# Kernel tuning notes

Measured on AMD Instinct MI355X. Metric: run time of the kernel, lower is better.

The kernel has to match this reference:

```python
import jax, jax.numpy as jnp
import numpy as np

P = 100_000      # distinct products
T = 300_000      # total product nodes after repeat_interleave (sum of cnt)
NQ = 100_000     # query nodes
B = 8192         # number of sessions (segments)
QIN = 128; PIN = 128; D = 128; MSL = 50; DL = D - MSL


def setup_inputs() -> dict:
    key = jax.random.key(0)
    ks = jax.random.split(key, 12)
    # irregular repeat counts in {1..5}, tiled so sum == 3*P == T exactly (static shape)
    cnt = jnp.asarray(np.tile(np.array([1, 2, 3, 4, 5], np.int32), P // 5))
    s = 0.05
    return {
        "query_feat": jax.random.normal(ks[0], (NQ, QIN), jnp.float32),
        "product_feat": jax.random.normal(ks[1], (P, PIN), jnp.float32),
        "Wq": jax.random.normal(ks[2], (DL, QIN), jnp.float32) * s,
        "bq": jnp.zeros((DL,), jnp.float32),
        "Wp": jax.random.normal(ks[3], (DL, PIN), jnp.float32) * s,
        "bp": jnp.zeros((DL,), jnp.float32),
        "pos_table": jax.random.normal(ks[4], (MSL, MSL), jnp.float32) * s,
        "Wn": jax.random.normal(ks[5], (D, D), jnp.float32) * s,
        "bn": jnp.zeros((D,), jnp.float32),
        "Wc": jax.random.normal(ks[6], (D, D), jnp.float32) * s,
        "Wa": jax.random.normal(ks[7], (1, D), jnp.float32) * s,
        "query_pos_id": jax.random.randint(ks[8], (NQ,), 0, MSL, jnp.int32),
        "product_pos_id": jax.random.randint(ks[9], (T,), 0, MSL, jnp.int32),
        "query_batch": jax.random.randint(ks[10], (NQ,), 0, B, jnp.int32),
        "product_batch": jax.random.randint(ks[11], (P,), 0, B, jnp.int32),
        "cnt": cnt,
        "num_segments": B,
        "total_product_nodes": T,
    }


def _segment_mean(x, seg, num_segments):
    sums = jax.ops.segment_sum(x, seg, num_segments=num_segments)
    counts = jax.ops.segment_sum(jnp.ones((x.shape[0],), x.dtype), seg, num_segments=num_segments)
    return sums / jnp.maximum(counts, 1.0)[:, None]


def reference(query_feat, product_feat, Wq, bq, Wp, bp, pos_table, Wn, bn, Wc, Wa,
              query_pos_id, product_pos_id, query_batch, product_batch, cnt,
              num_segments, total_product_nodes):
    # query branch: linear -> concat positional embedding -> tanh  [NQ, D]
    qe = jnp.tanh(jnp.concatenate([query_feat @ Wq.T + bq, pos_table[query_pos_id]], axis=1))
    # product branch: linear, repeat_interleave by cnt, concat pos emb, tanh  [T, D]
    pe = product_feat @ Wp.T + bp
    pe = jnp.repeat(pe, cnt, axis=0, total_repeat_length=total_product_nodes)
    pe = jnp.tanh(jnp.concatenate([pe, pos_table[product_pos_id]], axis=1))
    pbatch = jnp.repeat(product_batch, cnt, axis=0, total_repeat_length=total_product_nodes)
    # stack nodes (products first, then queries — matches torch.concat order)
    node_emb = jnp.concatenate([pe, qe], axis=0)            # [N, D]
    node_batch = jnp.concatenate([pbatch, query_batch], axis=0)
    # coarse session representation: segment mean, broadcast back to nodes
    coarse = _segment_mean(node_emb, node_batch, num_segments)  # [B, D]
    coarse_g = coarse[node_batch]                                # [N, D]
    # attention gating
    att = jax.nn.sigmoid(node_emb @ Wn.T + bn + coarse_g @ Wc.T) @ Wa.T  # [N, 1]
    weighted = node_emb * att
    return _segment_mean(weighted, node_batch, num_segments)    # [B, D]
```

## Files before the change

### kernel.cpp

```cpp
#include <hip/hip_runtime.h>
#include <hip/hip_bf16.h>
#include <math.h>


constexpr int D   = 128;
constexpr int DL  = 78;
constexpr int MSL = 50;
constexpr int RP  = 80;

typedef __attribute__((ext_vector_type(8))) short bfrag8;
typedef __attribute__((ext_vector_type(4))) float facc4;
typedef __attribute__((ext_vector_type(4))) short short4v;

__device__ __forceinline__ float sigmoidf_(float x) {
    return 1.f / (1.f + __expf(-x));
}
__device__ __forceinline__ float ftanh(float x) {
    float e = __expf(2.f * x);
    return 1.f - 2.f * __builtin_amdgcn_rcpf(e + 1.f);
}
__device__ __forceinline__ float bs2f(short s) {
    unsigned u = ((unsigned)(unsigned short)s) << 16;
    return __builtin_bit_cast(float, u);
}
__device__ __forceinline__ short f2bs(float f) {
    return __builtin_bit_cast(short, __float2bfloat16(f));
}

__device__ __forceinline__ char* ldsAddr(__hip_bfloat16* base, int row, int byte_in_row) {
    return reinterpret_cast<char*>(base) + row * 256 + (byte_in_row ^ ((row & 7) << 4));
}
__device__ __forceinline__ bfrag8 ldsR16(const __hip_bfloat16* base, int row, int byte_in_row) {
    return *reinterpret_cast<const bfrag8*>(
        reinterpret_cast<const char*>(base) + row * 256 + (byte_in_row ^ ((row & 7) << 4)));
}
__device__ __forceinline__ short4v ldsR8(const __hip_bfloat16* base, int row, int byte_in_row) {
    return *reinterpret_cast<const short4v*>(
        reinterpret_cast<const char*>(base) + row * 256 + (byte_in_row ^ ((row & 7) << 4)));
}

__device__ __forceinline__ bfrag8 cvt8(float4 a, float4 b) {
    __hip_bfloat16 t[8] = {__float2bfloat16(a.x), __float2bfloat16(a.y),
                           __float2bfloat16(a.z), __float2bfloat16(a.w),
                           __float2bfloat16(b.x), __float2bfloat16(b.y),
                           __float2bfloat16(b.z), __float2bfloat16(b.w)};
    return *reinterpret_cast<bfrag8*>(t);
}

__global__ __launch_bounds__(256) void k_tables2(
    const float* __restrict__ pos_table, const float* __restrict__ Wn,
    float* __restrict__ tpos, __hip_bfloat16* __restrict__ posWnbf) {
    __shared__ float tposL[MSL * MSL];
    int t = threadIdx.x;
    for (int o = t; o < MSL * MSL; o += 256) tposL[o] = tanhf(pos_table[o]);
    __syncthreads();
    if (blockIdx.x == 0)
        for (int o = t; o < MSL * MSL; o += 256) tpos[o] = tposL[o];
    for (int o = blockIdx.x * 256 + t; o < MSL * D; o += gridDim.x * 256) {
        int r = o >> 7, d = o & 127;
        float acc = 0.f;
        #pragma unroll 10
        for (int j = 0; j < MSL; ++j) acc += tposL[r * MSL + j] * Wn[d * D + DL + j];
        posWnbf[o] = __float2bfloat16(acc);
    }
}

__global__ __launch_bounds__(256) void k_convW(
    const float* __restrict__ Wq, const float* __restrict__ Wp, const float* __restrict__ Wn,
    const float* __restrict__ Wa,
    __hip_bfloat16* __restrict__ Wqbf, __hip_bfloat16* __restrict__ Wpbf,
    __hip_bfloat16* __restrict__ Wnbf, __hip_bfloat16* __restrict__ Wabf) {
    int i = blockIdx.x * 256 + threadIdx.x;
    if (i < 80 * 128) {
        int n = i >> 7;
        Wqbf[i] = __float2bfloat16((n < DL) ? Wq[i] : 0.f);
        Wpbf[i] = __float2bfloat16((n < DL) ? Wp[i] : 0.f);
    } else if (i < 80 * 128 + 128 * 128) {
        int o = i - 80 * 128;
        int j = o & 127;
        Wnbf[o] = __float2bfloat16((j < DL) ? Wn[o] : 0.f);
    } else if (i < 80 * 128 + 128 * 128 + 128) {
        int o = i - 80 * 128 - 128 * 128;
        Wabf[o] = __float2bfloat16(Wa[o]);
    }
}

__global__ void k_scanA(const int* __restrict__ cnt, int P, int* __restrict__ chunkSum) {
    __shared__ int s[256];
    int p = blockIdx.x * 256 + threadIdx.x;
    s[threadIdx.x] = (p < P) ? cnt[p] : 0;
    __syncthreads();
    for (int st = 128; st > 0; st >>= 1) {
        if (threadIdx.x < st) s[threadIdx.x] += s[threadIdx.x + st];
        __syncthreads();
    }
    if (threadIdx.x == 0) chunkSum[blockIdx.x] = s[0];
}
__global__ __launch_bounds__(1024) void k_scanB(
    const int* __restrict__ chunkSum, int nC, int* __restrict__ chunkOff) {
    __shared__ int s[1024];
    int t = threadIdx.x;
    int carry = 0;
    for (int base = 0; base < nC; base += 1024) {
        int v = (base + t < nC) ? chunkSum[base + t] : 0;
        s[t] = v;
        __syncthreads();
        for (int st = 1; st < 1024; st <<= 1) {
            int add = (t >= st) ? s[t - st] : 0;
            __syncthreads();
            s[t] += add;
            __syncthreads();
        }
        if (base + t < nC) chunkOff[base + t] = carry + s[t] - v;
        carry += s[1023];
        __syncthreads();
    }
}
__global__ void k_scanC(const int* __restrict__ cnt, int P, const int* __restrict__ chunkOff,
                        int* __restrict__ prodOff) {
    __shared__ int s[256];
    int t = threadIdx.x;
    int p = blockIdx.x * 256 + t;
    int v = (p < P) ? cnt[p] : 0;
    s[t] = v;
    __syncthreads();
    for (int st = 1; st < 256; st <<= 1) {
        int add = (t >= st) ? s[t - st] : 0;
        __syncthreads();
        s[t] += add;
        __syncthreads();
    }
    if (p < P) prodOff[p] = chunkOff[blockIdx.x] + s[t] - v;
}

__global__ void k_cnt2(const int* __restrict__ qbatch, const int* __restrict__ pbatch,
                       const int* __restrict__ cnt, int NQ, int P, int* __restrict__ nodeCnt) {
    int i = blockIdx.x * 256 + threadIdx.x;
    if (i < NQ) {
        atomicAdd(&nodeCnt[qbatch[i]], 1);
    } else if (i < NQ + P) {
        int p = i - NQ;
        atomicAdd(&nodeCnt[pbatch[p]], cnt[p]);
    }
}
__global__ __launch_bounds__(1024) void k_scanSeg(
    const int* __restrict__ nodeCnt, int B, int* __restrict__ segOff, int* __restrict__ cursor) {
    __shared__ int s[1024];
    int t = threadIdx.x;
    int carry = 0;
    for (int base = 0; base < B; base += 1024) {
        int v = (base + t < B) ? nodeCnt[base + t] : 0;
        s[t] = v;
        __syncthreads();
        for (int st = 1; st < 1024; st <<= 1) {
            int add = (t >= st) ? s[t - st] : 0;
            __syncthreads();
            s[t] += add;
            __syncthreads();
        }
        if (base + t < B) {
            int e = carry + s[t] - v;
            segOff[base + t] = e;
            cursor[base + t] = e;
        }
        carry += s[1023];
        __syncthreads();
    }
    if (t == 0) segOff[B] = carry;
}
__global__ void k_rank2(const int* __restrict__ qbatch, const int* __restrict__ pbatch,
                        const int* __restrict__ qpos, const int* __restrict__ ppos,
                        const int* __restrict__ cnt, const int* __restrict__ prodOff,
                        int NQ, int P, int* __restrict__ cursor,
                        int* __restrict__ nodeIdx, int* __restrict__ nodeSeg) {
    int i = blockIdx.x * 256 + threadIdx.x;
    if (i < NQ) {
        int b = qbatch[i];
        int slot = atomicAdd(&cursor[b], 1);
        nodeIdx[slot] = (i << 6) | qpos[i];
        nodeSeg[slot] = b;
    } else if (i < NQ + P) {
        int p = i - NQ;
        int b = pbatch[p];
        int c = cnt[p], off = prodOff[p];
        int slot = atomicAdd(&cursor[b], c);
        for (int j = 0; j < c; ++j) {
            nodeIdx[slot + j] = ((NQ + p) << 6) | ppos[off + j];
            nodeSeg[slot + j] = b;
        }
    }
}

__global__ __launch_bounds__(256) void k_branch2(
    const float* __restrict__ qfeat, const float* __restrict__ pfeat,
    const __hip_bfloat16* __restrict__ Wqbf, const __hip_bfloat16* __restrict__ Wpbf,
    const float* __restrict__ bq, const float* __restrict__ bp,
    const __hip_bfloat16* __restrict__ Wnbf,
    int NQ, int P, int qBlocks,
    __hip_bfloat16* __restrict__ tEU, __hip_bfloat16* __restrict__ eWnU) {
    const bool isQ = (int)blockIdx.x < qBlocks;
    const int r0 = (isQ ? blockIdx.x : blockIdx.x - qBlocks) * 64;
    const float* feat = isQ ? qfeat : pfeat;
    const __hip_bfloat16* Wbf = isQ ? Wqbf : Wpbf;
    const float* bias = isQ ? bq : bp;
    const int Nrows = isQ ? NQ : P;
    const int rowBase = isQ ? 0 : NQ;

    __shared__ __hip_bfloat16 linL[64 * 128];
    __shared__ __hip_bfloat16 eWnL[64 * 128];
    int t = threadIdx.x;
    int l = t & 63, w = t >> 6;
    int lr = l & 15, lq = l >> 4;
    int am = w * 16 + lr;

    if (l < 16) {
        bfrag8 z = {0, 0, 0, 0, 0, 0, 0, 0};
        *reinterpret_cast<bfrag8*>(ldsAddr(linL, w * 16 + l, 160)) = z;
        *reinterpret_cast<bfrag8*>(ldsAddr(linL, w * 16 + l, 176)) = z;
    }

    int gra = r0 + am;
    const float* frow = &feat[(size_t)(gra < Nrows ? gra : Nrows - 1) * 128];
    bfrag8 a[4];
    #pragma unroll
    for (int kt = 0; kt < 4; ++kt) {
        float4 u = *reinterpret_cast<const float4*>(&frow[kt * 32 + lq * 8]);
        float4 v = *reinterpret_cast<const float4*>(&frow[kt * 32 + lq * 8 + 4]);
        a[kt] = cvt8(u, v);
    }

    facc4 c1[5];
    #pragma unroll
    for (int nt = 0; nt < 5; ++nt) { facc4 z = {0.f, 0.f, 0.f, 0.f}; c1[nt] = z; }
    #pragma unroll
    for (int nt = 0; nt < 5; ++nt) {
        #pragma unroll
        for (int kt = 0; kt < 4; ++kt) {
            bfrag8 b = *reinterpret_cast<const bfrag8*>(&Wbf[(nt * 16 + lr) * 128 + kt * 32 + lq * 8]);
            c1[nt] = __builtin_amdgcn_mfma_f32_16x16x32_bf16(a[kt], b, c1[nt], 0, 0, 0);
        }
    }

    #pragma unroll
    for (int nt = 0; nt < 5; ++nt) {
        int n = nt * 16 + lr;
        float bs = (n < DL) ? bias[n] : 0.f;
        #pragma unroll
        for (int j = 0; j < 4; ++j) {
            int m = w * 16 + lq * 4 + j;
            float tv = (n < DL) ? ftanh(c1[nt][j] + bs) : 0.f;
            *reinterpret_cast<__hip_bfloat16*>(ldsAddr(linL, m, 2 * n)) = __float2bfloat16(tv);
        }
    }

    {
        int r = w * 16 + (l >> 2), c = l & 3;
        int gr = r0 + r;
        #pragma unroll
        for (int j = 0; j < 5; ++j) {
            short4v v = ldsR8(linL, r, c * 40 + j * 8);
            if (gr < Nrows)
                *reinterpret_cast<short4v*>(&tEU[(size_t)(rowBase + gr) * RP + c * 20 + j * 4]) = v;
        }
    }

    bfrag8 a2[3];
    #pragma unroll
    for (int kt = 0; kt < 3; ++kt) a2[kt] = ldsR16(linL, am, kt * 64 + lq * 16);
    facc4 c2[8];
    #pragma unroll
    for (int nt = 0; nt < 8; ++nt) { facc4 z = {0.f, 0.f, 0.f, 0.f}; c2[nt] = z; }
    #pragma unroll
    for (int nt = 0; nt < 8; ++nt) {
        #pragma unroll
        for (int kt = 0; kt < 3; ++kt) {
            bfrag8 b = *reinterpret_cast<const bfrag8*>(&Wnbf[(nt * 16 + lr) * 128 + kt * 32 + lq * 8]);
            c2[nt] = __builtin_amdgcn_mfma_f32_16x16x32_bf16(a2[kt], b, c2[nt], 0, 0, 0);
        }
    }
    #pragma unroll
    for (int nt = 0; nt < 8; ++nt) {
        int d2 = nt * 16 + lr;
        #pragma unroll
        for (int j = 0; j < 4; ++j) {
            int m = w * 16 + lq * 4 + j;
            *reinterpret_cast<__hip_bfloat16*>(ldsAddr(eWnL, m, 2 * d2)) =
                __float2bfloat16(c2[nt][j]);
        }
    }
    {
        int r = w * 16 + (l >> 2), c = l & 3;
        int gr = r0 + r;
        #pragma unroll
        for (int j = 0; j < 4; ++j) {
            bfrag8 v = ldsR16(eWnL, r, c * 64 + j * 16);
            if (gr < Nrows)
                *reinterpret_cast<bfrag8*>(&eWnU[(size_t)(rowBase + gr) * 128 + c * 32 + j * 8]) = v;
        }
    }
}

__global__ __launch_bounds__(128) void k_segsum3(
    const __hip_bfloat16* __restrict__ tEU, const int* __restrict__ nodeIdx,
    const int* __restrict__ segOff, const float* __restrict__ tpos, int B,
    float* __restrict__ segsum, float* __restrict__ segcnt) {
    int b = blockIdx.x, t = threadIdx.x;
    int s0 = segOff[b], s1 = segOff[b + 1];
    float acc = 0.f;
    if (t < DL) {
        for (int i = s0; i < s1; i += 4) {
            #pragma unroll
            for (int j = 0; j < 4; ++j) {
                if (i + j < s1) {
                    int row = nodeIdx[i + j] >> 6;
                    acc += __bfloat162float(tEU[(size_t)row * RP + t]);
                }
            }
        }
        segsum[(size_t)b * D + t] = acc;
    } else {
        int k = t - DL;
        for (int i = s0; i < s1; i += 4) {
            #pragma unroll
            for (int j = 0; j < 4; ++j) {
                if (i + j < s1) {
                    int pos = nodeIdx[i + j] & 63;
                    acc += tpos[pos * MSL + k];
                }
            }
        }
        segsum[(size_t)b * D + DL + k] = acc;
        if (k == 0) segcnt[b] = (float)(s1 - s0);
    }
}

__global__ __launch_bounds__(256) void k_coarse(
    const float* __restrict__ segsum, const float* __restrict__ segcnt,
    const float* __restrict__ Wc, const float* __restrict__ bn, int B,
    __hip_bfloat16* __restrict__ cWcbf) {
    __shared__ __hip_bfloat16 WcL[128 * 130];
    __shared__ float cL[16 * 128];
    int t = threadIdx.x;
    int b0 = blockIdx.x * 16;
    for (int o = t; o < D * D; o += 256) {
        int d = o >> 7, k = o & 127;
        WcL[d * 130 + k] = __float2bfloat16(Wc[o]);
    }
    for (int o = t; o < 16 * D; o += 256) {
        int bb = o >> 7, d = o & 127;
        int b = b0 + bb;
        cL[o] = (b < B) ? segsum[(size_t)b * D + d] / fmaxf(segcnt[b], 1.f) : 0.f;
    }
    __syncthreads();
    for (int o = t; o < 16 * D; o += 256) {
        int bb = o >> 7, d = o & 127;
        int b = b0 + bb;
        if (b >= B) continue;
        float acc = bn[d];
        const float* cr = &cL[bb * 128];
        const __hip_bfloat16* wr = &WcL[d * 130];
        #pragma unroll 8
        for (int j = 0; j < D; ++j) acc += cr[j] * __bfloat162float(wr[j]);
        cWcbf[(size_t)b * D + d] = __float2bfloat16(acc);
    }
}

__global__ __launch_bounds__(256) void k_attw(
    const __hip_bfloat16* __restrict__ eWnU, const __hip_bfloat16* __restrict__ cWcbf,
    const __hip_bfloat16* __restrict__ posWnbf, const __hip_bfloat16* __restrict__ Wabf,
    const int* __restrict__ nodeIdx, const int* __restrict__ nodeSeg,
    int NN, float* __restrict__ att) {
    int t = threadIdx.x;
    int l = t & 63, w = t >> 6;
    int lr = l & 15, lq = l >> 4;
    int i0 = blockIdx.x * 64 + w * 16;
    int n = i0 + lr;
    bool on = n < NN;
    int pk = on ? nodeIdx[n] : 0;
    int b  = on ? nodeSeg[n] : 0;
    int row = pk >> 6, pos = pk & 63;

    facc4 c = {0.f, 0.f, 0.f, 0.f};
    #pragma unroll
    for (int kt = 0; kt < 4; ++kt) {
        int col = kt * 32 + lq * 8;
        bfrag8 e  = *reinterpret_cast<const bfrag8*>(&eWnU[(size_t)row * D + col]);
        bfrag8 cw = *reinterpret_cast<const bfrag8*>(&cWcbf[(size_t)b * D + col]);
        bfrag8 pw = *reinterpret_cast<const bfrag8*>(&posWnbf[pos * D + col]);
        bfrag8 s;
        #pragma unroll
        for (int j = 0; j < 8; ++j) {
            float z = bs2f(e[j]) + bs2f(cw[j]) + bs2f(pw[j]);
            s[j] = f2bs(sigmoidf_(z));
        }
        bfrag8 wa = *reinterpret_cast<const bfrag8*>(&Wabf[col]);
        c = __builtin_amdgcn_mfma_f32_16x16x32_bf16(s, wa, c, 0, 0, 0);
    }
    if (lr == 0) {
        #pragma unroll
        for (int j = 0; j < 4; ++j) {
            int m = i0 + lq * 4 + j;
            if (m < NN) att[m] = c[j];
        }
    }
}

__global__ __launch_bounds__(256) void k_pool(
    const __hip_bfloat16* __restrict__ tEU, const float* __restrict__ att,
    const float* __restrict__ tpos, const int* __restrict__ nodeIdx,
    const int* __restrict__ segOff, const float* __restrict__ segcnt,
    int B, float* __restrict__ out) {
    int wv = threadIdx.x >> 6, l = threadIdx.x & 63;
    int b = blockIdx.x * 4 + wv;
    if (b >= B) return;
    int s0 = segOff[b], s1 = segOff[b + 1];
    float acc0 = 0.f, acc1 = 0.f;

    for (int i = s0; i < s1; i += 4) {
        float a[4];
        int row[4], pos[4];
        #pragma unroll
        for (int j = 0; j < 4; ++j) {
            bool on = (i + j) < s1;
            int pk = on ? nodeIdx[i + j] : 0;
            a[j] = on ? att[i + j] : 0.f;
            row[j] = pk >> 6;
            pos[j] = pk & 63;
        }
        #pragma unroll
        for (int j = 0; j < 4; ++j) {
            acc0 += a[j] * __bfloat162float(tEU[(size_t)row[j] * RP + l]);
            if (l < 14) acc1 += a[j] * __bfloat162float(tEU[(size_t)row[j] * RP + 64 + l]);
            else        acc1 += a[j] * tpos[pos[j] * MSL + (l - 14)];
        }
    }

    float inv = 1.f / fmaxf(segcnt[b], 1.f);
    out[(size_t)b * D + l] = acc0 * inv;
    out[(size_t)b * D + 64 + l] = acc1 * inv;
}

extern "C" void kernel_launch(void* const* d_in, const int* in_sizes, int n_in,
                              void* d_out, int out_size, void* d_ws, size_t ws_size,
                              hipStream_t stream) {
    const float* query_feat   = (const float*)d_in[0];
    const float* product_feat = (const float*)d_in[1];
    const float* Wq = (const float*)d_in[2];
    const float* bq = (const float*)d_in[3];
    const float* Wp = (const float*)d_in[4];
    const float* bp = (const float*)d_in[5];
    const float* pos_table = (const float*)d_in[6];
    const float* Wn = (const float*)d_in[7];
    const float* bn = (const float*)d_in[8];
    const float* Wc = (const float*)d_in[9];
    const float* Wa = (const float*)d_in[10];
    const int* qpos   = (const int*)d_in[11];
    const int* ppos   = (const int*)d_in[12];
    const int* qbatch = (const int*)d_in[13];
    const int* pbatch = (const int*)d_in[14];
    const int* cnt    = (const int*)d_in[15];

    int NQ = in_sizes[11];
    int T  = in_sizes[12];
    int P  = in_sizes[15];
    int B  = out_size / D;
    int NR = NQ + P;
    int NN = NQ + T;
    float* out = (float*)d_out;

    char* w = (char*)d_ws;
    size_t off = 0;
    auto take = [&](size_t bytes) -> char* {
        char* p = w + off;
        off = (off + bytes + 255) & ~(size_t)255;
        return p;
    };
    int*   nodeCnt = (int*)  take((size_t)B * 4);
    size_t zeroBytes = off;
    float* segsum   = (float*)take((size_t)B * D * 4);
    float* segcnt   = (float*)take((size_t)B * 4);
    float* tpos  = (float*)take(MSL * MSL * 4);
    __hip_bfloat16* posWnbf = (__hip_bfloat16*)take(MSL * D * 2);
    __hip_bfloat16* cWcbf   = (__hip_bfloat16*)take((size_t)B * D * 2);
    __hip_bfloat16* Wqbf = (__hip_bfloat16*)take(80 * 128 * 2);
    __hip_bfloat16* Wpbf = (__hip_bfloat16*)take(80 * 128 * 2);
    __hip_bfloat16* Wnbf = (__hip_bfloat16*)take(128 * 128 * 2);
    __hip_bfloat16* Wabf = (__hip_bfloat16*)take(128 * 2);
    int nC = (P + 255) / 256;
    int* chunkSum = (int*)take((size_t)nC * 4);
    int* chunkOff = (int*)take((size_t)nC * 4);
    int* prodOff  = (int*)take((size_t)P * 4);
    int* segOffA  = (int*)take((size_t)(B + 1) * 4);
    int* cursor   = (int*)take((size_t)B * 4);
    int* nodeIdx  = (int*)take((size_t)NN * 4);
    int* nodeSeg  = (int*)take((size_t)NN * 4);
    float* att    = (float*)take((size_t)NN * 4);
    __hip_bfloat16* tEU  = (__hip_bfloat16*)take((size_t)NR * RP * 2);
    __hip_bfloat16* eWnU = (__hip_bfloat16*)take((size_t)NR * D * 2);
    (void)ws_size; (void)n_in;

    hipMemsetAsync(nodeCnt, 0, zeroBytes, stream);

    hipLaunchKernelGGL(k_tables2, dim3(8), dim3(256), 0, stream, pos_table, Wn, tpos, posWnbf);
    hipLaunchKernelGGL(k_convW, dim3((80 * 128 + 128 * 128 + 128 + 255) / 256), dim3(256), 0,
                       stream, Wq, Wp, Wn, Wa, Wqbf, Wpbf, Wnbf, Wabf);
    hipLaunchKernelGGL(k_scanA, dim3(nC), dim3(256), 0, stream, cnt, P, chunkSum);
    hipLaunchKernelGGL(k_scanB, dim3(1), dim3(1024), 0, stream, chunkSum, nC, chunkOff);
    hipLaunchKernelGGL(k_scanC, dim3(nC), dim3(256), 0, stream, cnt, P, chunkOff, prodOff);

    hipLaunchKernelGGL(k_cnt2, dim3((NR + 255) / 256), dim3(256), 0, stream,
                       qbatch, pbatch, cnt, NQ, P, nodeCnt);
    hipLaunchKernelGGL(k_scanSeg, dim3(1), dim3(1024), 0, stream, nodeCnt, B, segOffA, cursor);
    hipLaunchKernelGGL(k_rank2, dim3((NR + 255) / 256), dim3(256), 0, stream,
                       qbatch, pbatch, qpos, ppos, cnt, prodOff, NQ, P, cursor,
                       nodeIdx, nodeSeg);

    int qBlocks = (NQ + 63) / 64, pBlocksBr = (P + 63) / 64;
    hipLaunchKernelGGL(k_branch2, dim3(qBlocks + pBlocksBr), dim3(256), 0, stream,
                       query_feat, product_feat, Wqbf, Wpbf, bq, bp, Wnbf,
                       NQ, P, qBlocks, tEU, eWnU);

    hipLaunchKernelGGL(k_segsum3, dim3(B), dim3(128), 0, stream,
                       tEU, nodeIdx, segOffA, tpos, B, segsum, segcnt);
    hipLaunchKernelGGL(k_coarse, dim3((B + 15) / 16), dim3(256), 0, stream,
                       segsum, segcnt, Wc, bn, B, cWcbf);

    hipLaunchKernelGGL(k_attw, dim3((NN + 63) / 64), dim3(256), 0, stream,
                       eWnU, cWcbf, posWnbf, Wabf, nodeIdx, nodeSeg, NN, att);
    hipLaunchKernelGGL(k_pool, dim3((B + 3) / 4), dim3(256), 0, stream,
                       tEU, att, tpos, nodeIdx, segOffA, segcnt, B, out);
}
```

Baseline: 322.8 us.

## Make branch kernel persistent with LDS-resident Wn and next-tile feature prefetch

The branch GEMM kernel becomes a persistent grid of 768 blocks that loops over 64-row tiles. Each block stages the bf16 Wn matrix in LDS once, and while the current tile computes it prefetches the next tile's fp32 feature rows into registers. A single LDS scratch buffer now replaces the separate linear and eWn buffers. The pooling kernel also unrolls its node loop from 4 to 8 to keep more gathers in flight. The aim is to amortise Wn loads and hide global feature-load latency, at the cost of more register pressure and fewer blocks in flight.

```diff
diff --git a/kernel.cpp b/kernel.cpp
--- a/kernel.cpp
+++ b/kernel.cpp
@@ -191,111 +191,145 @@
     }
 }
 
-__global__ __launch_bounds__(256) void k_branch2(
+__global__ __launch_bounds__(256) void k_branch3(
     const float* __restrict__ qfeat, const float* __restrict__ pfeat,
     const __hip_bfloat16* __restrict__ Wqbf, const __hip_bfloat16* __restrict__ Wpbf,
     const float* __restrict__ bq, const float* __restrict__ bp,
     const __hip_bfloat16* __restrict__ Wnbf,
-    int NQ, int P, int qBlocks,
+    int NQ, int P, int nTilesQ, int nTiles,
     __hip_bfloat16* __restrict__ tEU, __hip_bfloat16* __restrict__ eWnU) {
-    const bool isQ = (int)blockIdx.x < qBlocks;
-    const int r0 = (isQ ? blockIdx.x : blockIdx.x - qBlocks) * 64;
-    const float* feat = isQ ? qfeat : pfeat;
-    const __hip_bfloat16* Wbf = isQ ? Wqbf : Wpbf;
-    const float* bias = isQ ? bq : bp;
-    const int Nrows = isQ ? NQ : P;
-    const int rowBase = isQ ? 0 : NQ;
-
-    __shared__ __hip_bfloat16 linL[64 * 128];
-    __shared__ __hip_bfloat16 eWnL[64 * 128];
+    __shared__ __hip_bfloat16 sL[64 * 128];
+    __shared__ __hip_bfloat16 WnL[128 * 128];
+
     int t = threadIdx.x;
     int l = t & 63, w = t >> 6;
     int lr = l & 15, lq = l >> 4;
     int am = w * 16 + lr;
 
-    if (l < 16) {
-        bfrag8 z = {0, 0, 0, 0, 0, 0, 0, 0};
-        *reinterpret_cast<bfrag8*>(ldsAddr(linL, w * 16 + l, 160)) = z;
-        *reinterpret_cast<bfrag8*>(ldsAddr(linL, w * 16 + l, 176)) = z;
-    }
-
-    int gra = r0 + am;
-    const float* frow = &feat[(size_t)(gra < Nrows ? gra : Nrows - 1) * 128];
-    bfrag8 a[4];
-    #pragma unroll
-    for (int kt = 0; kt < 4; ++kt) {
-        float4 u = *reinterpret_cast<const float4*>(&frow[kt * 32 + lq * 8]);
-        float4 v = *reinterpret_cast<const float4*>(&frow[kt * 32 + lq * 8 + 4]);
-        a[kt] = cvt8(u, v);
-    }
-
-    facc4 c1[5];
-    #pragma unroll
-    for (int nt = 0; nt < 5; ++nt) { facc4 z = {0.f, 0.f, 0.f, 0.f}; c1[nt] = z; }
-    #pragma unroll
-    for (int nt = 0; nt < 5; ++nt) {
+    for (int i = t; i < 128 * 16; i += 256) {
+        int row = i >> 4, chunk = i & 15;
+        bfrag8 v = *reinterpret_cast<const bfrag8*>(&Wnbf[row * 128 + chunk * 8]);
+        *reinterpret_cast<bfrag8*>(ldsAddr(WnL, row, chunk * 16)) = v;
+    }
+    __syncthreads();
+
+    auto tileFrow = [&](int tl) -> const float* {
+        bool iq = tl < nTilesQ;
+        int r0 = (iq ? tl : tl - nTilesQ) * 64;
+        const float* f = iq ? qfeat : pfeat;
+        int Nr = iq ? NQ : P;
+        int gr = r0 + am;
+        return &f[(size_t)(gr < Nr ? gr : Nr - 1) * 128];
+    };
+
+    int tile = blockIdx.x;
+    float4 uN[4], vN[4];
+    if (tile < nTiles) {
+        const float* fr = tileFrow(tile);
         #pragma unroll
         for (int kt = 0; kt < 4; ++kt) {
-            bfrag8 b = *reinterpret_cast<const bfrag8*>(&Wbf[(nt * 16 + lr) * 128 + kt * 32 + lq * 8]);
-            c1[nt] = __builtin_amdgcn_mfma_f32_16x16x32_bf16(a[kt], b, c1[nt], 0, 0, 0);
-        }
-    }
-
-    #pragma unroll
-    for (int nt = 0; nt < 5; ++nt) {
-        int n = nt * 16 + lr;
-        float bs = (n < DL) ? bias[n] : 0.f;
-        #pragma unroll
-        for (int j = 0; j < 4; ++j) {
-            int m = w * 16 + lq * 4 + j;
-            float tv = (n < DL) ? ftanh(c1[nt][j] + bs) : 0.f;
-            *reinterpret_cast<__hip_bfloat16*>(ldsAddr(linL, m, 2 * n)) = __float2bfloat16(tv);
-        }
-    }
-
-    {
-        int r = w * 16 + (l >> 2), c = l & 3;
-        int gr = r0 + r;
-        #pragma unroll
-        for (int j = 0; j < 5; ++j) {
-            short4v v = ldsR8(linL, r, c * 40 + j * 8);
-            if (gr < Nrows)
-                *reinterpret_cast<short4v*>(&tEU[(size_t)(rowBase + gr) * RP + c * 20 + j * 4]) = v;
-        }
-    }
-
-    bfrag8 a2[3];
-    #pragma unroll
-    for (int kt = 0; kt < 3; ++kt) a2[kt] = ldsR16(linL, am, kt * 64 + lq * 16);
-    facc4 c2[8];
-    #pragma unroll
-    for (int nt = 0; nt < 8; ++nt) { facc4 z = {0.f, 0.f, 0.f, 0.f}; c2[nt] = z; }
-    #pragma unroll
-    for (int nt = 0; nt < 8; ++nt) {
-        #pragma unroll
-        for (int kt = 0; kt < 3; ++kt) {
-            bfrag8 b = *reinterpret_cast<const bfrag8*>(&Wnbf[(nt * 16 + lr) * 128 + kt * 32 + lq * 8]);
-            c2[nt] = __builtin_amdgcn_mfma_f32_16x16x32_bf16(a2[kt], b, c2[nt], 0, 0, 0);
-        }
-    }
-    #pragma unroll
-    for (int nt = 0; nt < 8; ++nt) {
-        int d2 = nt * 16 + lr;
-        #pragma unroll
-        for (int j = 0; j < 4; ++j) {
-            int m = w * 16 + lq * 4 + j;
-            *reinterpret_cast<__hip_bfloat16*>(ldsAddr(eWnL, m, 2 * d2)) =
-                __float2bfloat16(c2[nt][j]);
-        }
-    }
-    {
-        int r = w * 16 + (l >> 2), c = l & 3;
-        int gr = r0 + r;
-        #pragma unroll
-        for (int j = 0; j < 4; ++j) {
-            bfrag8 v = ldsR16(eWnL, r, c * 64 + j * 16);
-            if (gr < Nrows)
-                *reinterpret_cast<bfrag8*>(&eWnU[(size_t)(rowBase + gr) * 128 + c * 32 + j * 8]) = v;
+            uN[kt] = *reinterpret_cast<const float4*>(&fr[kt * 32 + lq * 8]);
+            vN[kt] = *reinterpret_cast<const float4*>(&fr[kt * 32 + lq * 8 + 4]);
+        }
+    }
+
+    for (; tile < nTiles; tile += gridDim.x) {
+        const bool isQ = tile < nTilesQ;
+        const int r0 = (isQ ? tile : tile - nTilesQ) * 64;
+        const __hip_bfloat16* Wbf = isQ ? Wqbf : Wpbf;
+        const float* bias = isQ ? bq : bp;
+        const int Nrows = isQ ? NQ : P;
+        const int rowBase = isQ ? 0 : NQ;
+
+        bfrag8 a[4];
+        #pragma unroll
+        for (int kt = 0; kt < 4; ++kt) a[kt] = cvt8(uN[kt], vN[kt]);
+
+        if (l < 16) {
+            bfrag8 z = {0, 0, 0, 0, 0, 0, 0, 0};
+            *reinterpret_cast<bfrag8*>(ldsAddr(sL, w * 16 + l, 160)) = z;
+            *reinterpret_cast<bfrag8*>(ldsAddr(sL, w * 16 + l, 176)) = z;
+        }
+
+        facc4 c1[5];
+        #pragma unroll
+        for (int nt = 0; nt < 5; ++nt) { facc4 z = {0.f, 0.f, 0.f, 0.f}; c1[nt] = z; }
+        #pragma unroll
+        for (int nt = 0; nt < 5; ++nt) {
+            #pragma unroll
+            for (int kt = 0; kt < 4; ++kt) {
+                bfrag8 b = *reinterpret_cast<const bfrag8*>(&Wbf[(nt * 16 + lr) * 128 + kt * 32 + lq * 8]);
+                c1[nt] = __builtin_amdgcn_mfma_f32_16x16x32_bf16(a[kt], b, c1[nt], 0, 0, 0);
+            }
+        }
+
+        int tnext = tile + gridDim.x;
+        if (tnext < nTiles) {
+            const float* fr = tileFrow(tnext);
+            #pragma unroll
+            for (int kt = 0; kt < 4; ++kt) {
+                uN[kt] = *reinterpret_cast<const float4*>(&fr[kt * 32 + lq * 8]);
+                vN[kt] = *reinterpret_cast<const float4*>(&fr[kt * 32 + lq * 8 + 4]);
+            }
+        }
+
+        #pragma unroll
+        for (int nt = 0; nt < 5; ++nt) {
+            int n = nt * 16 + lr;
+            float bs = (n < DL) ? bias[n] : 0.f;
+            #pragma unroll
+            for (int j = 0; j < 4; ++j) {
+                int m = w * 16 + lq * 4 + j;
+                float tv = (n < DL) ? ftanh(c1[nt][j] + bs) : 0.f;
+                *reinterpret_cast<__hip_bfloat16*>(ldsAddr(sL, m, 2 * n)) = __float2bfloat16(tv);
+            }
+        }
+
+        {
+            int r = w * 16 + (l >> 2), c = l & 3;
+            int gr = r0 + r;
+            #pragma unroll
+            for (int j = 0; j < 5; ++j) {
+                short4v v = ldsR8(sL, r, c * 40 + j * 8);
+                if (gr < Nrows)
+                    *reinterpret_cast<short4v*>(&tEU[(size_t)(rowBase + gr) * RP + c * 20 + j * 4]) = v;
+            }
+        }
+
+        bfrag8 a2[3];
+        #pragma unroll
+        for (int kt = 0; kt < 3; ++kt) a2[kt] = ldsR16(sL, am, kt * 64 + lq * 16);
+        facc4 c2[8];
+        #pragma unroll
+        for (int nt = 0; nt < 8; ++nt) { facc4 z = {0.f, 0.f, 0.f, 0.f}; c2[nt] = z; }
+        #pragma unroll
+        for (int nt = 0; nt < 8; ++nt) {
+            #pragma unroll
+            for (int kt = 0; kt < 3; ++kt) {
+                bfrag8 b = ldsR16(WnL, nt * 16 + lr, kt * 64 + lq * 16);
+                c2[nt] = __builtin_amdgcn_mfma_f32_16x16x32_bf16(a2[kt], b, c2[nt], 0, 0, 0);
+            }
+        }
+
+        #pragma unroll
+        for (int nt = 0; nt < 8; ++nt) {
+            int d2 = nt * 16 + lr;
+            #pragma unroll
+            for (int j = 0; j < 4; ++j) {
+                int m = w * 16 + lq * 4 + j;
+                *reinterpret_cast<__hip_bfloat16*>(ldsAddr(sL, m, 2 * d2)) =
+                    __float2bfloat16(c2[nt][j]);
+            }
+        }
+        {
+            int r = w * 16 + (l >> 2), c = l & 3;
+            int gr = r0 + r;
+            #pragma unroll
+            for (int j = 0; j < 4; ++j) {
+                bfrag8 v = ldsR16(sL, r, c * 64 + j * 16);
+                if (gr < Nrows)
+                    *reinterpret_cast<bfrag8*>(&eWnU[(size_t)(rowBase + gr) * 128 + c * 32 + j * 8]) = v;
+            }
         }
     }
 }
@@ -416,11 +450,11 @@
     int s0 = segOff[b], s1 = segOff[b + 1];
     float acc0 = 0.f, acc1 = 0.f;
 
-    for (int i = s0; i < s1; i += 4) {
-        float a[4];
-        int row[4], pos[4];
-        #pragma unroll
-        for (int j = 0; j < 4; ++j) {
+    for (int i = s0; i < s1; i += 8) {
+        float a[8];
+        int row[8], pos[8];
+        #pragma unroll
+        for (int j = 0; j < 8; ++j) {
             bool on = (i + j) < s1;
             int pk = on ? nodeIdx[i + j] : 0;
             a[j] = on ? att[i + j] : 0.f;
@@ -428,7 +462,7 @@
             pos[j] = pk & 63;
         }
         #pragma unroll
-        for (int j = 0; j < 4; ++j) {
+        for (int j = 0; j < 8; ++j) {
             acc0 += a[j] * __bfloat162float(tEU[(size_t)row[j] * RP + l]);
             if (l < 14) acc1 += a[j] * __bfloat162float(tEU[(size_t)row[j] * RP + 64 + l]);
             else        acc1 += a[j] * tpos[pos[j] * MSL + (l - 14)];
@@ -515,10 +549,10 @@
                        qbatch, pbatch, qpos, ppos, cnt, prodOff, NQ, P, cursor,
                        nodeIdx, nodeSeg);
 
-    int qBlocks = (NQ + 63) / 64, pBlocksBr = (P + 63) / 64;
-    hipLaunchKernelGGL(k_branch2, dim3(qBlocks + pBlocksBr), dim3(256), 0, stream,
+    int nTilesQ = (NQ + 63) / 64, nTilesP = (P + 63) / 64;
+    hipLaunchKernelGGL(k_branch3, dim3(768), dim3(256), 0, stream,
                        query_feat, product_feat, Wqbf, Wpbf, bq, bp, Wnbf,
-                       NQ, P, qBlocks, tEU, eWnU);
+                       NQ, P, nTilesQ, nTilesQ + nTilesP, tEU, eWnU);
 
     hipLaunchKernelGGL(k_segsum3, dim3(B), dim3(128), 0, stream,
                        tEU, nodeIdx, segOffA, tpos, B, segsum, segcnt);
```

Result: faster. 312.5 us (-3.2%).
